# Performance work log

Measured on AMD Instinct MI355X. Metric: run time of the kernel, lower is better.

Reference implementation:

```python
import jax, jax.numpy as jnp
import numpy as np

HID, HEADS = 2048, 16
HD = HID // HEADS  # head_dim = 128
EPS = 1e-6


def rope_tables(head_dim, max_pos, base=10000.0):
    inv = 1.0 / (base ** (jnp.arange(0, head_dim, 2, dtype=jnp.float32) / head_dim))
    t = jnp.arange(max_pos, dtype=jnp.float32)
    freqs = jnp.outer(t, inv)                      # [max_pos, d/2]
    emb = jnp.concatenate([freqs, freqs], axis=-1)  # [max_pos, d]
    return jnp.cos(emb), jnp.sin(emb)


def rotate_half(x):
    x1, x2 = jnp.split(x, 2, axis=-1)
    return jnp.concatenate([-x2, x1], axis=-1)


def lf_gate(x, c1w, c1b, c2w, c2b, rms_w):
    # x: [b, s, h]; prompt phase -> lf1/lf2 caches are zeros -> zero-pad 1 step on time axis
    xt = jnp.transpose(x, (0, 2, 1))[..., None]                 # [b, h, s, 1]
    xt = jnp.pad(xt, ((0, 0), (0, 0), (1, 0), (0, 0)))           # [b, h, s+1, 1]
    dn = ('NCHW', 'OIHW', 'NCHW')
    o1 = jax.lax.conv_general_dilated(xt, c1w, (1, 1), 'VALID', dimension_numbers=dn)
    o1 = o1 + c1b[None, :, None, None]                           # [b, h/2, s, 1]
    o1 = jnp.pad(o1, ((0, 0), (0, 0), (1, 0), (0, 0)))           # [b, h/2, s+1, 1]
    o2 = jax.lax.conv_general_dilated(o1, c2w, (1, 1), 'VALID', dimension_numbers=dn)
    o2 = o2 + c2b[None, :, None, None]                           # [b, h, s, 1]
    y = jnp.transpose(o2[..., 0], (0, 2, 1)) + x                 # residual, [b, s, h]
    var = jnp.mean(y * y, axis=-1, keepdims=True)
    return y * jax.lax.rsqrt(var + EPS) * rms_w


def setup_inputs() -> dict:
    key = jax.random.key(0)
    ks = jax.random.split(key, 10)
    b, s = 2, 2048
    inp = {
        'hidden_states': jax.random.normal(ks[0], (b, s, HID), jnp.float32),
        'positions': jnp.arange(s, dtype=jnp.int32),
        'wq': jax.random.normal(ks[1], (HID, HID), jnp.float32) * 0.02,
        'wk': jax.random.normal(ks[2], (HID, HID), jnp.float32) * 0.02,
        'wv': jax.random.normal(ks[3], (HID, HID), jnp.float32) * 0.02,
        'wo': jax.random.normal(ks[4], (HID, HID), jnp.float32) * 0.02,
        'conv1_w': jax.random.normal(ks[5], (HID // 2, HID, 2, 1), jnp.float32) * 0.02,
        'conv1_b': jnp.zeros((HID // 2,), jnp.float32),
        'conv2_w': jax.random.normal(ks[6], (HID, HID // 2, 2, 1), jnp.float32) * 0.02,
        'conv2_b': jnp.zeros((HID,), jnp.float32),
        'rms_w': jnp.ones((HID,), jnp.float32),
    }
    return inp


def reference(hidden_states, positions, wq, wk, wv, wo, conv1_w, conv1_b, conv2_w, conv2_b, rms_w):
    b, s, _ = hidden_states.shape
    # value projection from raw hidden states (pre-gate)
    v = (hidden_states @ wv).reshape(b, s, HEADS, HD)            # [b, s, H, d]
    # localized-filtering gate (prompt phase: zero caches)
    h = lf_gate(hidden_states, conv1_w, conv1_b, conv2_w, conv2_b, rms_w)
    q = h @ wq                                                   # [b, s, H*d]
    k = h @ wk
    # faithful Yuan quirk: concat q,k then reshape to [b,s,H,2d] and chunk
    qk = jnp.concatenate([q, k], axis=-1).reshape(b, s, HEADS, 2 * HD)
    q, k = jnp.split(qk, 2, axis=-1)                             # each [b, s, H, d]
    # rotary
    cos, sin = rope_tables(HD, 8192)
    c = cos[positions][None, :, None, :]                         # [1, s, 1, d]
    sn = sin[positions][None, :, None, :]
    q = q * c + rotate_half(q) * sn
    k = k * c + rotate_half(k) * sn
    # causal attention (paged attention reduces to this for the prompt)
    scale = HD ** -0.5
    scores = jnp.einsum('bqhd,bkhd->bhqk', q, k) * scale         # [b, H, s, s]
    mask = jnp.tril(jnp.ones((s, s), dtype=bool))
    scores = jnp.where(mask[None, None], scores, jnp.finfo(scores.dtype).min)
    probs = jax.nn.softmax(scores, axis=-1)
    out = jnp.einsum('bhqk,bkhd->bqhd', probs, v).reshape(b, s, HEADS * HD)
    return out @ wo
```

## Files before the change

### kernel.cpp

```cpp
#include <hip/hip_runtime.h>

#define HID 2048
#define HEADS 16
#define HD 128
#define BATCH 2
#define S 2048
#define ROWS (BATCH*S)

typedef short short8 __attribute__((ext_vector_type(8)));
typedef unsigned short ushort4v __attribute__((ext_vector_type(4)));
typedef unsigned short ushort2v __attribute__((ext_vector_type(2)));
typedef float f32x4 __attribute__((ext_vector_type(4)));
typedef __bf16 bf16x8 __attribute__((ext_vector_type(8)));
typedef __bf16 bf16x4 __attribute__((ext_vector_type(4)));

static __device__ __forceinline__ float b2f(unsigned short u) {
  union { float f; unsigned int i; } v; v.i = ((unsigned int)u) << 16; return v.f;
}
static __device__ __forceinline__ unsigned short f2b(float f) {
  union { float f; unsigned int i; } v; v.f = f;
  unsigned int u = v.i;
  unsigned int r = ((u >> 16) & 1u) + 0x7fffu;
  return (unsigned short)((u + r) >> 16);
}

static __device__ __forceinline__ void gload_lds16(const unsigned short* g, unsigned short* l) {
  __builtin_amdgcn_global_load_lds(
      (const __attribute__((address_space(1))) unsigned int*)(const void*)g,
      (__attribute__((address_space(3))) unsigned int*)(void*)l,
      16, 0, 0);
}

__global__ void fill_debug(unsigned short* __restrict__ out, long n) {
  long i = (long)blockIdx.x * blockDim.x + threadIdx.x;
  if (i < n) out[i] = 0x447A;
}

__global__ void prep_all(const float* __restrict__ c1w, const float* __restrict__ c2w,
                         const float* __restrict__ x, const int* __restrict__ positions,
                         const float* __restrict__ c1b, const float* __restrict__ c2b,
                         const float* __restrict__ rmsw,
                         unsigned short* __restrict__ w1t0, unsigned short* __restrict__ w1t1,
                         unsigned short* __restrict__ w2t0, unsigned short* __restrict__ w2t1,
                         unsigned short* __restrict__ xb,
                         float* __restrict__ ctab, float* __restrict__ stab,
                         unsigned short* __restrict__ c1bb, unsigned short* __restrict__ c2bb,
                         unsigned short* __restrict__ rmswb, unsigned short* __restrict__ zpg) {
  int job = blockIdx.y;
  if (job == 0 || job == 1) {
    const float* w = (job == 0) ? c1w : c2w;
    unsigned short* o0 = (job == 0) ? w1t0 : w2t0;
    unsigned short* o1 = (job == 0) ? w1t1 : w2t1;
    long i = (long)blockIdx.x * 256 + threadIdx.x;
    f32x4 v = *(const f32x4*)(w + i*4);
    ushort2v a = { f2b(v[0]), f2b(v[2]) };
    ushort2v b = { f2b(v[1]), f2b(v[3]) };
    *(ushort2v*)(o0 + i*2) = a;
    *(ushort2v*)(o1 + i*2) = b;
  } else if (job == 2) {
    long i = (long)blockIdx.x * 256 + threadIdx.x;
    #pragma unroll
    for (int rep = 0; rep < 2; ++rep) {
      long idx = i + (long)rep * 1048576L;
      f32x4 v = *(const f32x4*)(x + idx*4);
      ushort4v o = { f2b(v[0]), f2b(v[1]), f2b(v[2]), f2b(v[3]) };
      *(ushort4v*)(xb + idx*4) = o;
    }
  } else {
    int bx = blockIdx.x;
    if (bx < 512) {
      int t = bx * 4 + (threadIdx.x >> 6);
      int i = threadIdx.x & 63;
      float pos = (float)positions[t];
      float inv = powf(10000.0f, -(float)i / 64.0f);
      float ang = pos * inv;
      float sv, cv;
      sincosf(ang, &sv, &cv);
      ctab[t*64 + i] = cv;
      stab[t*64 + i] = sv;
    } else if (bx < 544) {
      int i = (bx - 512) * 256 + threadIdx.x;
      if (i < 1024) c1bb[i] = f2b(c1b[i]);
      if (i < 2048) { c2bb[i] = f2b(c2b[i]); rmswb[i] = f2b(rmsw[i]); }
      zpg[i] = 0;
    }
  }
}

__global__ void transpose4(const float* __restrict__ s0, const float* __restrict__ s1,
                           const float* __restrict__ s2, const float* __restrict__ s3,
                           unsigned short* __restrict__ d0, unsigned short* __restrict__ d1,
                           unsigned short* __restrict__ d2, unsigned short* __restrict__ d3) {
  __shared__ unsigned short tl[64][73];
  const float* in; unsigned short* out; int perm;
  switch (blockIdx.z) {
    case 0:  in = s0; out = d0; perm = 1; break;
    case 1:  in = s1; out = d1; perm = 1; break;
    case 2:  in = s2; out = d2; perm = 0; break;
    default: in = s3; out = d3; perm = 0; break;
  }
  int n0 = blockIdx.x * 64, k0 = blockIdx.y * 64;
  int tid = threadIdx.x;
  int r = tid >> 3, c8 = (tid & 7) * 8;
  #pragma unroll
  for (int j = 0; j < 2; ++j) {
    int rr = r + j*32;
    const float* p = in + (size_t)(k0 + rr)*HID + n0 + c8;
    f32x4 v0 = *(const f32x4*)p;
    f32x4 v1 = *(const f32x4*)(p + 4);
    #pragma unroll
    for (int e = 0; e < 4; ++e) { tl[rr][c8 + e] = f2b(v0[e]); tl[rr][c8 + 4 + e] = f2b(v1[e]); }
  }
  __syncthreads();
  #pragma unroll
  for (int j = 0; j < 2; ++j) {
    int rr = r + j*32;
    int orow = n0 + rr;
    if (perm) {
      int s5 = (orow >> 5) & 3;
      s5 = (s5 == 1) ? 2 : (s5 == 2) ? 1 : s5;
      orow = (orow & ~127) | (s5 << 5) | (orow & 31);
    }
    short8 v;
    #pragma unroll
    for (int e = 0; e < 8; ++e) v[e] = (short)tl[c8 + e][rr];
    *(short8*)(out + (size_t)orow*HID + k0 + c8) = v;
  }
}


static __device__ __forceinline__ int swz_scol(int lane) {
  return (((lane & 7) * 16) ^ (((lane >> 3) & 7) << 4)) >> 1;
}

static __device__ __forceinline__ void rd_af(const unsigned short* Ah, bf16x8 (&afr)[4][2],
                                             int wm, int lr, int col0, int axor) {
  #pragma unroll
  for (int mi = 0; mi < 4; ++mi) {
    const unsigned short* rp = Ah + (wm*64 + mi*16 + lr) * 64;
    #pragma unroll
    for (int kk = 0; kk < 2; ++kk)
      afr[mi][kk] = *(const bf16x8*)(rp + (((kk*64 + col0) ^ axor) >> 1));
  }
}
static __device__ __forceinline__ void rd_bf(const unsigned short* Bh, bf16x8 (&bfr)[2][2],
                                             int wn, int lr, int col0, int axor) {
  #pragma unroll
  for (int ni = 0; ni < 2; ++ni) {
    const unsigned short* rp = Bh + (wn*32 + ni*16 + lr) * 64;
    #pragma unroll
    for (int kk = 0; kk < 2; ++kk)
      bfr[ni][kk] = *(const bf16x8*)(rp + (((kk*64 + col0) ^ axor) >> 1));
  }
}
static __device__ __forceinline__ void mfma16(const bf16x8 (&afr)[4][2], const bf16x8 (&bfr)[2][2],
                                              f32x4 (&ac)[4][2]) {
  #pragma unroll
  for (int kk = 0; kk < 2; ++kk)
    #pragma unroll
    for (int mi = 0; mi < 4; ++mi)
      #pragma unroll
      for (int ni = 0; ni < 2; ++ni)
        ac[mi][ni] = __builtin_amdgcn_mfma_f32_16x16x32_bf16(afr[mi][kk], bfr[ni][kk], ac[mi][ni], 0, 0, 0);
}


struct SPtrs { const unsigned short* p[6]; };

static __device__ __forceinline__ void build_ptrs(SPtrs& sp,
    const unsigned short* Ap, const unsigned short* Bp, int Ksz, int sh,
    int m0, int n0, const unsigned short* zpg, int tid) {
  int lane = tid & 63;
  int scol = swz_scol(lane);
  #pragma unroll
  for (int j = 0; j < 2; ++j) {
    int row = ((tid >> 6) * 2 + j) * 8 + (lane >> 3);
    int gr = m0 + row;
    sp.p[j]     = (sh && ((gr & (S - 1)) == 0)) ? (zpg + scol)
                                                : (Ap + (size_t)(gr - sh)*Ksz + scol);
    sp.p[2 + j] = Bp + (size_t)(n0 + row)*Ksz + scol;
    sp.p[4 + j] = Bp + (size_t)(n0 + 128 + row)*Ksz + scol;
  }
}

static __device__ __forceinline__ void stage6(unsigned short* buf, SPtrs& sp, int tid) {
  int c0 = (tid >> 6) * 1024;
  gload_lds16(sp.p[0], buf + c0);
  gload_lds16(sp.p[1], buf + c0 + 512);
  gload_lds16(sp.p[2], buf + 8192  + c0);
  gload_lds16(sp.p[3], buf + 8192  + c0 + 512);
  gload_lds16(sp.p[4], buf + 16384 + c0);
  gload_lds16(sp.p[5], buf + 16384 + c0 + 512);
  #pragma unroll
  for (int i = 0; i < 6; ++i) sp.p[i] += 64;
}

static __device__ __forceinline__ void gemm8_core(
    unsigned short* lds,
    const unsigned short* __restrict__ A1, const unsigned short* __restrict__ A2,
    const unsigned short* __restrict__ B1, const unsigned short* __restrict__ B2,
    int K1, int K2,
    const unsigned short* __restrict__ bias, const unsigned short* __restrict__ resid,
    void* __restrict__ Cout, int outmode, int N, int m0, int n0,
    int a1shift, const unsigned short* __restrict__ zrow) {
  int tid = threadIdx.x;
  int lane = tid & 63, w = tid >> 6;
  int wm = w >> 2, wn = w & 3;
  int lr = lane & 15, g = lane >> 4;
  int col0 = g * 16;
  int axor = (lr & 7) << 4;
  int nk1 = K1 >> 6;
  int nk = (K1 + K2) >> 6;
  f32x4 acc[2][4][2] = {};
  bf16x8 afr[4][2], bfr0[2][2], bfr1[2][2];

  unsigned short* buf0 = lds;
  unsigned short* buf1 = lds + 24576;
  unsigned short* buf2 = lds + 49152;

  SPtrs sp;
  build_ptrs(sp, A1, B1, K1, a1shift, m0, n0, zrow, tid);

  stage6(buf0, sp, tid);
  stage6(buf1, sp, tid);

  unsigned short* cur = buf0;
  unsigned short* nx1 = buf1;
  unsigned short* nx2 = buf2;
  for (int t = 0; t < nk; ++t) {
    if (t < nk - 1) asm volatile("s_waitcnt vmcnt(6)" ::: "memory");
    else            asm volatile("s_waitcnt vmcnt(0)" ::: "memory");
    __builtin_amdgcn_s_barrier();
    asm volatile("" ::: "memory");

    rd_af(cur,         afr,  wm, lr, col0, axor);
    rd_bf(cur + 8192,  bfr0, wn, lr, col0, axor);
    rd_bf(cur + 16384, bfr1, wn, lr, col0, axor);
    if (t + 2 < nk) {
      if (t + 2 == nk1) build_ptrs(sp, A2, B2, K2, 0, m0, n0, zrow, tid);
      stage6(nx2, sp, tid);
    }
    __builtin_amdgcn_s_setprio(1);
    mfma16(afr, bfr0, acc[0]);
    mfma16(afr, bfr1, acc[1]);
    __builtin_amdgcn_s_setprio(0);

    unsigned short* tmp = cur; cur = nx1; nx1 = nx2; nx2 = tmp;
  }

  #pragma unroll
  for (int qn = 0; qn < 2; ++qn)
    #pragma unroll
    for (int mi = 0; mi < 4; ++mi) {
      int row0 = m0 + wm*64 + mi*16 + g*4;
      #pragma unroll
      for (int ni = 0; ni < 2; ++ni) {
        int col = n0 + qn*128 + wn*32 + ni*16 + lr;
        float bv = bias ? b2f(bias[col]) : 0.f;
        f32x4 a = acc[qn][mi][ni];
        #pragma unroll
        for (int j = 0; j < 4; ++j) {
          size_t idx = (size_t)(row0 + j) * N + col;
          float v = a[j] + bv;
          if (resid) v += b2f(resid[idx]);
          if (outmode == 1) ((float*)Cout)[idx] = v;
          else ((unsigned short*)Cout)[idx] = f2b(v);
        }
      }
    }
}

template<int SHIFT>
__launch_bounds__(512, 1)
__global__ void gemm8_bt(const unsigned short* __restrict__ A1,
                         const unsigned short* __restrict__ A2,
                         const unsigned short* __restrict__ B1,
                         const unsigned short* __restrict__ B2,
                         int K1, int K2,
                         const unsigned short* __restrict__ bias,
                         const unsigned short* __restrict__ resid,
                         void* __restrict__ Cout, int outmode, int N,
                         const unsigned short* __restrict__ zrow) {
  __shared__ __align__(16) unsigned short lds[73728];
  gemm8_core(lds, A1, A2, B1, B2, K1, K2, bias, resid, Cout, outmode, N,
             blockIdx.x*128, blockIdx.y*256, SHIFT, zrow);
}

struct HPtr { const unsigned short* p0; const unsigned short* p1; };
static __device__ __forceinline__ void hinit(HPtr& h, const unsigned short* base,
                                             int row0, int tid) {
  int lane = tid & 63;
  int scol = swz_scol(lane);
  int r0 = ((tid >> 6) * 2) * 8 + (lane >> 3);
  h.p0 = base + (size_t)(row0 + r0) * 2048 + scol;
  h.p1 = base + (size_t)(row0 + r0 + 8) * 2048 + scol;
}
static __device__ __forceinline__ void hinit_sh(HPtr& h, const unsigned short* base,
                                                int row0, const unsigned short* zpg, int tid) {
  int lane = tid & 63;
  int scol = swz_scol(lane);
  int r0 = ((tid >> 6) * 2) * 8 + (lane >> 3);
  int g0 = row0 + r0, g1 = row0 + r0 + 8;
  h.p0 = ((g0 & (S - 1)) == 0) ? (zpg + scol) : (base + (size_t)(g0 - 1) * 2048 + scol);
  h.p1 = ((g1 & (S - 1)) == 0) ? (zpg + scol) : (base + (size_t)(g1 - 1) * 2048 + scol);
}
static __device__ __forceinline__ void hstage(unsigned short* slot, HPtr& h, int tid) {
  int c0 = (tid >> 6) * 1024;
  gload_lds16(h.p0, slot + c0);
  gload_lds16(h.p1, slot + c0 + 512);
  h.p0 += 64; h.p1 += 64;
}

static __device__ __forceinline__ void gemm256_loop(
    unsigned short* lds, HPtr& hA0, HPtr& hA1, HPtr& hB0, HPtr& hB1,
    f32x4 (&acc)[2][2][4][2], int wm, int wn, int lr, int col0, int axor, int tid) {
  bf16x8 af[4][2], bf0[2][2], bf1[2][2];
  const int nk = 2048 >> 6;
  hstage(lds + 0,             hA0, tid);
  hstage(lds + 8192,          hA1, tid);
  hstage(lds + 16384,         hB0, tid);
  hstage(lds + 24576,         hB1, tid);
  hstage(lds + 32768 + 0,     hA0, tid);
  hstage(lds + 32768 + 16384, hB0, tid);
  hstage(lds + 32768 + 24576, hB1, tid);
  asm volatile("s_waitcnt vmcnt(6)" ::: "memory");
  __builtin_amdgcn_s_barrier();
  asm volatile("" ::: "memory");

  for (int t = 0; t < nk; ++t) {
    unsigned short* cur = lds + (t & 1) * 32768;
    unsigned short* oth = lds + ((t & 1) ^ 1) * 32768;

    rd_af(cur,         af,  wm, lr, col0, axor);
    rd_bf(cur + 16384, bf0, wn, lr, col0, axor);
    if (t + 1 < nk) hstage(oth + 8192, hA1, tid);
    __builtin_amdgcn_s_barrier();
    asm volatile("s_waitcnt lgkmcnt(0)" ::: "memory");
    __builtin_amdgcn_s_setprio(1);
    mfma16(af, bf0, acc[0][0]);
    __builtin_amdgcn_s_setprio(0);
    __builtin_amdgcn_s_barrier();

    rd_bf(cur + 24576, bf1, wn, lr, col0, axor);
    if (t + 2 < nk) hstage(cur, hA0, tid);
    __builtin_amdgcn_s_barrier();
    asm volatile("s_waitcnt lgkmcnt(0)" ::: "memory");
    __builtin_amdgcn_s_setprio(1);
    mfma16(af, bf1, acc[0][1]);
    __builtin_amdgcn_s_setprio(0);
    __builtin_amdgcn_s_barrier();

    rd_af(cur + 8192, af, wm, lr, col0, axor);
    if (t + 2 < nk) hstage(cur + 16384, hB0, tid);
    __builtin_amdgcn_s_barrier();
    asm volatile("s_waitcnt lgkmcnt(0)" ::: "memory");
    __builtin_amdgcn_s_setprio(1);
    mfma16(af, bf1, acc[1][1]);
    __builtin_amdgcn_s_setprio(0);
    __builtin_amdgcn_s_barrier();

    if (t + 2 < nk) hstage(cur + 24576, hB1, tid);
    __builtin_amdgcn_s_barrier();
    asm volatile("s_waitcnt lgkmcnt(0)" ::: "memory");
    __builtin_amdgcn_s_setprio(1);
    mfma16(af, bf0, acc[1][0]);
    __builtin_amdgcn_s_setprio(0);
    if (t + 2 < nk) asm volatile("s_waitcnt vmcnt(6)" ::: "memory");
    else            asm volatile("s_waitcnt vmcnt(0)" ::: "memory");
    __builtin_amdgcn_s_barrier();
    asm volatile("" ::: "memory");
  }
}

__launch_bounds__(512, 1)
__global__ void gemm256_bt(const unsigned short* __restrict__ A,
                           const unsigned short* __restrict__ B,
                           unsigned short* __restrict__ C, int N) {
  __shared__ __align__(16) unsigned short lds[65536];
  int tid = threadIdx.x;
  int lane = tid & 63, w = tid >> 6;
  int wm = w >> 2, wn = w & 3;
  int lr = lane & 15, g = lane >> 4;
  int col0 = g * 16;
  int axor = (lr & 7) << 4;
  int nwg = gridDim.x * gridDim.y;
  int lin = blockIdx.y * gridDim.x + blockIdx.x;
  int cpx = nwg >> 3;
  int swz = (lin & 7) * cpx + (lin >> 3);
  int m0 = (swz % gridDim.x) * 256, n0 = (swz / gridDim.x) * 256;
  f32x4 acc[2][2][4][2] = {};

  HPtr hA0, hA1, hB0, hB1;
  hinit(hA0, A, m0,       tid);
  hinit(hA1, A, m0 + 128, tid);
  hinit(hB0, B, n0,       tid);
  hinit(hB1, B, n0 + 128, tid);
  gemm256_loop(lds, hA0, hA1, hB0, hB1, acc, wm, wn, lr, col0, axor, tid);

  #pragma unroll
  for (int qm = 0; qm < 2; ++qm)
    #pragma unroll
    for (int mi = 0; mi < 4; ++mi) {
      int row0 = m0 + qm*128 + wm*64 + mi*16 + g*4;
      #pragma unroll
      for (int qn = 0; qn < 2; ++qn)
        #pragma unroll
        for (int ni = 0; ni < 2; ++ni) {
          int col = n0 + qn*128 + wn*32 + ni*16 + lr;
          f32x4 a = acc[qm][qn][mi][ni];
          #pragma unroll
          for (int j = 0; j < 4; ++j)
            C[(size_t)(row0 + j) * N + col] = f2b(a[j]);
        }
    }
}

__launch_bounds__(512, 1)
__global__ void gemm256_trio(const unsigned short* __restrict__ xb,
                             const unsigned short* __restrict__ w1t0,
                             const unsigned short* __restrict__ w1t1,
                             const unsigned short* __restrict__ wvt,
                             unsigned short* __restrict__ o1a,
                             unsigned short* __restrict__ o1b,
                             unsigned short* __restrict__ vtg,
                             const unsigned short* __restrict__ zpg) {
  __shared__ __align__(16) unsigned short lds[65536];
  int tid = threadIdx.x;
  int lane = tid & 63, w = tid >> 6;
  int wm = w >> 2, wn = w & 3;
  int lr = lane & 15, g = lane >> 4;
  int col0 = g * 16;
  int axor = (lr & 7) << 4;
  int lin = blockIdx.x;
  int swz = (lin & 7) * 32 + (lin >> 3);
  int job, s;
  if (swz < 64)       { job = 0; s = swz; }
  else if (swz < 128) { job = 1; s = swz - 64; }
  else                { job = 2; s = swz - 128; }
  int m0 = (s & 15) * 256;
  int n0 = (s >> 4) * 256;
  f32x4 acc[2][2][4][2] = {};

  HPtr hA0, hA1, hB0, hB1;
  if (job == 0) { hinit_sh(hA0, xb, m0, zpg, tid); hinit_sh(hA1, xb, m0 + 128, zpg, tid); }
  else          { hinit(hA0, xb, m0, tid);         hinit(hA1, xb, m0 + 128, tid); }
  const unsigned short* B = (job == 0) ? w1t0 : (job == 1) ? w1t1 : wvt;
  hinit(hB0, B, n0,       tid);
  hinit(hB1, B, n0 + 128, tid);
  gemm256_loop(lds, hA0, hA1, hB0, hB1, acc, wm, wn, lr, col0, axor, tid);

  if (job < 2) {
    unsigned short* C = (job == 0) ? o1a : o1b;
    #pragma unroll
    for (int qm = 0; qm < 2; ++qm)
      #pragma unroll
      for (int mi = 0; mi < 4; ++mi) {
        int row0 = m0 + qm*128 + wm*64 + mi*16 + g*4;
        #pragma unroll
        for (int qn = 0; qn < 2; ++qn)
          #pragma unroll
          for (int ni = 0; ni < 2; ++ni) {
            int col = n0 + qn*128 + wn*32 + ni*16 + lr;
            f32x4 a = acc[qm][qn][mi][ni];
            #pragma unroll
            for (int j = 0; j < 4; ++j)
              C[(size_t)(row0 + j) * 1024 + col] = f2b(a[j]);
          }
      }
  } else {
    #pragma unroll
    for (int qm = 0; qm < 2; ++qm)
      #pragma unroll
      for (int mi = 0; mi < 4; ++mi) {
        int row0 = m0 + qm*128 + wm*64 + mi*16 + g*4;
        int bb = row0 >> 11;
        int s0 = row0 & (S - 1);
        #pragma unroll
        for (int qn = 0; qn < 2; ++qn)
          #pragma unroll
          for (int ni = 0; ni < 2; ++ni) {
            int col = n0 + qn*128 + wn*32 + ni*16 + lr;
            size_t base = ((size_t)bb * HID + col) * S + s0;
            f32x4 a = acc[qm][qn][mi][ni];
            ushort4v pk;
            #pragma unroll
            for (int j = 0; j < 4; ++j) pk[j] = f2b(a[j]);
            *(ushort4v*)(vtg + base) = pk;
          }
      }
  }
}

__global__ void add_bias(const unsigned short* __restrict__ a,
                         const unsigned short* __restrict__ b,
                         const unsigned short* __restrict__ bias,
                         unsigned short* __restrict__ o) {
  long i8 = ((long)blockIdx.x * 256 + threadIdx.x) * 8;
  short8 va = *(const short8*)(a + i8);
  short8 vb = *(const short8*)(b + i8);
  short8 wb = *(const short8*)(bias + (i8 & 1023));
  short8 vo;
  #pragma unroll
  for (int e = 0; e < 8; ++e)
    vo[e] = (short)f2b(b2f((unsigned short)va[e]) + b2f((unsigned short)vb[e])
                       + b2f((unsigned short)wb[e]));
  *(short8*)(o + i8) = vo;
}

__global__ void rmsnorm_rows(const unsigned short* __restrict__ y,
                             const unsigned short* __restrict__ w,
                             unsigned short* __restrict__ out) {
  int r = blockIdx.x;
  int c8 = threadIdx.x * 8;
  const unsigned short* yr = y + (size_t)r * HID;
  short8 v = *(const short8*)(yr + c8);
  float f[8];
  float ss = 0.f;
  #pragma unroll
  for (int e = 0; e < 8; ++e) { f[e] = b2f((unsigned short)v[e]); ss += f[e]*f[e]; }
  #pragma unroll
  for (int o = 32; o; o >>= 1) ss += __shfl_xor(ss, o);
  __shared__ float red[4];
  if ((threadIdx.x & 63) == 0) red[threadIdx.x >> 6] = ss;
  __syncthreads();
  float tot = red[0] + red[1] + red[2] + red[3];
  float scale = rsqrtf(tot / (float)HID + 1e-6f);
  short8 wv = *(const short8*)(w + c8);
  short8 o8;
  #pragma unroll
  for (int e = 0; e < 8; ++e) o8[e] = (short)f2b(f[e] * scale * b2f((unsigned short)wv[e]));
  *(short8*)(out + (size_t)r*HID + c8) = o8;
}

__global__ void rope_rearrange(const unsigned short* __restrict__ qkf,
                               const float* __restrict__ ctab, const float* __restrict__ stab,
                               unsigned short* __restrict__ qr, unsigned short* __restrict__ kr) {
  int r = blockIdx.x;
  int t = r & (S - 1);
  int h = threadIdx.x >> 4;
  int i4 = (threadIdx.x & 15) * 4;
  int pc = (i4 & 31) + ((i4 >> 5) << 6);
  const unsigned short* qk = qkf + (size_t)r * (2*HID) + h * 256;
  f32x4 c = *(const f32x4*)(ctab + t*64 + i4);
  f32x4 s = *(const f32x4*)(stab + t*64 + i4);
  ushort4v q1 = *(const ushort4v*)(qk + pc);
  ushort4v q2 = *(const ushort4v*)(qk + pc + 32);
  ushort4v k1 = *(const ushort4v*)(qk + 128 + pc);
  ushort4v k2 = *(const ushort4v*)(qk + 128 + pc + 32);
  size_t o = (size_t)r * HID + (size_t)h * HD;
  const float SC = 0.08838834764831845f * 1.44269504088896340f;
  ushort4v oq1, oq2, ok1, ok2;
  #pragma unroll
  for (int e = 0; e < 4; ++e) {
    float a = b2f(q1[e]), b = b2f(q2[e]);
    float x = b2f(k1[e]), y = b2f(k2[e]);
    oq1[e] = f2b((a*c[e] - b*s[e]) * SC);
    oq2[e] = f2b((b*c[e] + a*s[e]) * SC);
    ok1[e] = f2b(x*c[e] - y*s[e]);
    ok2[e] = f2b(y*c[e] + x*s[e]);
  }
  *(ushort4v*)(qr + o + i4)      = oq1;
  *(ushort4v*)(qr + o + 64 + i4) = oq2;
  *(ushort4v*)(kr + o + i4)      = ok1;
  *(ushort4v*)(kr + o + 64 + i4) = ok2;
}

#define KT 64

static __device__ __forceinline__ void attn_pass(
    int qt, int b, int h, unsigned short* lds,
    const unsigned short* __restrict__ Qr, const unsigned short* __restrict__ Kr,
    const unsigned short* __restrict__ Vt, unsigned short* __restrict__ Out) {
  int tid = threadIdx.x, lane = tid & 63, w = tid >> 6;
  int q0 = qt * 64;
  size_t bS = (size_t)b * S;
  size_t ho = (size_t)h * HD;
  int lr = lane & 15, g = lane >> 4;
  int rsw = (lane & 7) << 3;
  __syncthreads();
  bf16x8 bq[4];
  {
    int qrow = q0 + w*16 + lr;
    const unsigned short* qp = Qr + (bS + qrow)*HID + ho + g*8;
    #pragma unroll
    for (int kk = 0; kk < 4; ++kk) bq[kk] = *(const bf16x8*)(qp + kk*32);
  }
  const unsigned short* kp[4];
  const unsigned short* vp[4];
  #pragma unroll
  for (int j = 0; j < 4; ++j) {
    int c = w*4 + j;
    int rk = c*4 + (lane >> 4);
    int sck = ((lane & 15) * 8) ^ ((rk & 7) << 3);
    kp[j] = Kr + (bS + rk)*HID + ho + sck;
    int rv = c*8 + (lane >> 3);
    int scv = ((lane & 7) * 8) ^ ((rv & 7) << 3);
    vp[j] = Vt + ((size_t)b*HID + ho + rv)*S + scv;
  }
  int cdst = (w*4) * 512;
  unsigned short* curK = lds;
  unsigned short* curV = lds + 8192;
  unsigned short* nxtK = lds + 16384;
  unsigned short* nxtV = lds + 24576;
  #pragma unroll
  for (int j = 0; j < 4; ++j) {
    gload_lds16(kp[j], curK + cdst + j*512);
    gload_lds16(vp[j], curV + cdst + j*512);
    kp[j] += (size_t)KT * HID;
    vp[j] += KT;
  }
  f32x4 o[8] = {};
  float m = -1e30f, l = 0.f;
  unsigned short* PlW = lds + 32768 + w*1024;
  int ntiles = qt + 1;
  for (int kt = 0; kt < ntiles; ++kt) {
    asm volatile("s_waitcnt vmcnt(0)" ::: "memory");
    __builtin_amdgcn_s_barrier();
    asm volatile("" ::: "memory");
    if (kt + 1 < ntiles) {
      #pragma unroll
      for (int j = 0; j < 4; ++j) {
        gload_lds16(kp[j], nxtK + cdst + j*512);
        gload_lds16(vp[j], nxtV + cdst + j*512);
        kp[j] += (size_t)KT * HID;
        vp[j] += KT;
      }
    }
    f32x4 st[4] = {};
    __builtin_amdgcn_s_setprio(1);
    #pragma unroll
    for (int kk = 0; kk < 4; ++kk) {
      #pragma unroll
      for (int mi = 0; mi < 4; ++mi) {
        bf16x8 a = *(const bf16x8*)(&curK[(mi*16 + lr)*128 + ((kk*32 + g*8) ^ rsw)]);
        st[mi] = __builtin_amdgcn_mfma_f32_16x16x32_bf16(a, bq[kk], st[mi], 0, 0, 0);
      }
    }
    __builtin_amdgcn_s_setprio(0);
    bool lastt = (kt == ntiles - 1);
    float tm = -1e30f;
    #pragma unroll
    for (int mi = 0; mi < 4; ++mi)
      #pragma unroll
      for (int r = 0; r < 4; ++r) {
        float v = st[mi][r];
        if (lastt && (mi*16 + 4*g + r) > (w*16 + lr)) v = -1e30f;
        st[mi][r] = v;
        tm = fmaxf(tm, v);
      }
    tm = fmaxf(tm, __shfl_xor(tm, 16));
    tm = fmaxf(tm, __shfl_xor(tm, 32));
    if (!__all(tm - m <= 11.5f)) {
      float mn = fmaxf(m, tm);
      float sc = exp2f(m - mn);
      float s0 = __shfl(sc, 4*g+0), s1 = __shfl(sc, 4*g+1);
      float s2 = __shfl(sc, 4*g+2), s3 = __shfl(sc, 4*g+3);
      #pragma unroll
      for (int ni = 0; ni < 8; ++ni) {
        o[ni][0] *= s0; o[ni][1] *= s1; o[ni][2] *= s2; o[ni][3] *= s3;
      }
      l *= sc;
      m = mn;
    }
    float ts = 0.f;
    __bf16 pbf[4][4];
    #pragma unroll
    for (int mi = 0; mi < 4; ++mi)
      #pragma unroll
      for (int r = 0; r < 4; ++r) {
        float p = exp2f(st[mi][r] - m);
        ts += p;
        pbf[mi][r] = (__bf16)p;
      }
    ts += __shfl_xor(ts, 16);
    ts += __shfl_xor(ts, 32);
    l += ts;
    #pragma unroll
    for (int mi = 0; mi < 4; ++mi) {
      bf16x4 pk = { pbf[mi][0], pbf[mi][1], pbf[mi][2], pbf[mi][3] };
      *(bf16x4*)(&PlW[lr*64 + ((mi*16 + 4*g) ^ rsw)]) = pk;
    }
    asm volatile("" ::: "memory");
    __builtin_amdgcn_s_setprio(1);
    #pragma unroll
    for (int kk = 0; kk < 2; ++kk) {
      int pc = (kk*32 + g*8) ^ rsw;
      bf16x8 a = *(const bf16x8*)(&PlW[lr*64 + pc]);
      #pragma unroll
      for (int ni = 0; ni < 8; ++ni) {
        bf16x8 bv = *(const bf16x8*)(&curV[(ni*16 + lr)*64 + pc]);
        o[ni] = __builtin_amdgcn_mfma_f32_16x16x32_bf16(a, bv, o[ni], 0, 0, 0);
      }
    }
    __builtin_amdgcn_s_setprio(0);
    unsigned short* t0 = curK; curK = nxtK; nxtK = t0;
    unsigned short* t1 = curV; curV = nxtV; nxtV = t1;
  }
  float l0 = __shfl(l, 4*g+0), l1 = __shfl(l, 4*g+1);
  float l2 = __shfl(l, 4*g+2), l3 = __shfl(l, 4*g+3);
  float i0 = 1.f/l0, i1 = 1.f/l1, i2 = 1.f/l2, i3 = 1.f/l3;
  int rbase = q0 + w*16 + 4*g;
  #pragma unroll
  for (int ni = 0; ni < 8; ++ni) {
    size_t cbase = ho + ni*16 + lr;
    Out[(bS + rbase + 0)*HID + cbase] = f2b(o[ni][0]*i0);
    Out[(bS + rbase + 1)*HID + cbase] = f2b(o[ni][1]*i1);
    Out[(bS + rbase + 2)*HID + cbase] = f2b(o[ni][2]*i2);
    Out[(bS + rbase + 3)*HID + cbase] = f2b(o[ni][3]*i3);
  }
}

__launch_bounds__(256, 2)
__global__ void attn_mfma(const unsigned short* __restrict__ Qr,
                          const unsigned short* __restrict__ Kr,
                          const unsigned short* __restrict__ Vt,
                          unsigned short* __restrict__ Out) {
  __shared__ __align__(16) unsigned short lds[36864];
  int bh = blockIdx.x;
  int b = bh >> 4, h = bh & 15;
  int by = blockIdx.y;
  attn_pass(31 - by, b, h, lds, Qr, Kr, Vt, Out);
  attn_pass(by,      b, h, lds, Qr, Kr, Vt, Out);
}

extern "C" void kernel_launch(void* const* d_in, const int* in_sizes, int n_in,
                              void* d_out, int out_size, void* d_ws, size_t ws_size,
                              hipStream_t stream) {
  const float* x_raw   = (const float*)d_in[0];
  const int* positions = (const int*)d_in[1];
  const float* wq_raw  = (const float*)d_in[2];
  const float* wk_raw  = (const float*)d_in[3];
  const float* wv_raw  = (const float*)d_in[4];
  const float* wo_raw  = (const float*)d_in[5];
  const float* c1w_raw = (const float*)d_in[6];
  const float* c1b_raw = (const float*)d_in[7];
  const float* c2w_raw = (const float*)d_in[8];
  const float* c2b_raw = (const float*)d_in[9];
  const float* rms_raw = (const float*)d_in[10];

  const size_t WS_NEEDED = 140000000;
  if (ws_size < WS_NEEDED) {
    long n = (long)out_size;
    fill_debug<<<dim3((unsigned)((n + 255) / 256)), dim3(256), 0, stream>>>((unsigned short*)d_out, n);
    return;
  }

  char* ws = (char*)d_ws;
  size_t off = 0;
  auto alloc = [&](size_t bytes) { char* p = ws + off; off += (bytes + 255) & ~(size_t)255; return p; };
  float* ctab          = (float*)alloc((size_t)S*64*4);
  float* stab          = (float*)alloc((size_t)S*64*4);
  unsigned short* wqkt = (unsigned short*)alloc((size_t)2*HID*HID*2);
  unsigned short* wvt  = (unsigned short*)alloc((size_t)HID*HID*2);
  unsigned short* wot  = (unsigned short*)alloc((size_t)HID*HID*2);
  unsigned short* w1t0 = (unsigned short*)alloc((size_t)1024*HID*2);
  unsigned short* w1t1 = (unsigned short*)alloc((size_t)1024*HID*2);
  unsigned short* w2t0 = (unsigned short*)alloc((size_t)HID*1024*2);
  unsigned short* w2t1 = (unsigned short*)alloc((size_t)HID*1024*2);
  unsigned short* xb   = (unsigned short*)alloc((size_t)ROWS*HID*2);
  unsigned short* qrb  = (unsigned short*)alloc((size_t)ROWS*HID*2);
  unsigned short* o1   = (unsigned short*)alloc((size_t)ROWS*1024*2);
  unsigned short* yb   = (unsigned short*)alloc((size_t)ROWS*HID*2);
  unsigned short* hg   = (unsigned short*)alloc((size_t)ROWS*HID*2);
  unsigned short* qkf  = (unsigned short*)alloc((size_t)ROWS*2*HID*2);
  unsigned short* vtg  = (unsigned short*)alloc((size_t)BATCH*HID*S*2);
  unsigned short* c1bb = (unsigned short*)alloc(1024*2);
  unsigned short* c2bb = (unsigned short*)alloc(2048*2);
  unsigned short* rmswb= (unsigned short*)alloc(2048*2);
  unsigned short* zpg  = (unsigned short*)alloc(8192*2);
  unsigned short* krr  = xb;
  unsigned short* attn = yb;
  unsigned short* o1a  = qkf;
  unsigned short* o1b  = qkf + (size_t)ROWS*1024;

  dim3 b256(256);
  dim3 b512(512);
  prep_all<<<dim3(4096, 4), b256, 0, stream>>>(c1w_raw, c2w_raw, x_raw, positions,
                                               c1b_raw, c2b_raw, rms_raw,
                                               w1t0, w1t1, w2t0, w2t1, xb,
                                               ctab, stab, c1bb, c2bb, rmswb, zpg);
  transpose4<<<dim3(32,32,4), b256, 0, stream>>>(wq_raw, wk_raw, wv_raw, wo_raw,
                                                 wqkt, wqkt + (size_t)HID*HID, wvt, wot);
  gemm256_trio<<<dim3(256), b512, 0, stream>>>(xb, w1t0, w1t1, wvt, o1a, o1b, vtg, zpg);
  add_bias<<<dim3(ROWS*1024/8/256), b256, 0, stream>>>(o1a, o1b, c1bb, o1);
  gemm8_bt<1><<<dim3(ROWS/128, HID/256), b512, 0, stream>>>(o1, o1, w2t0, w2t1, 1024, 1024, c2bb, xb, yb, 0, HID, zpg);
  rmsnorm_rows<<<dim3(ROWS), b256, 0, stream>>>(yb, rmswb, hg);
  gemm256_bt<<<dim3(ROWS/256, (2*HID)/256), b512, 0, stream>>>(hg, wqkt, qkf, 2*HID);
  rope_rearrange<<<dim3(ROWS), b256, 0, stream>>>(qkf, ctab, stab, qrb, krr);
  attn_mfma<<<dim3(BATCH*HEADS, 16), b256, 0, stream>>>(qrb, krr, vtg, attn);
  gemm8_bt<0><<<dim3(ROWS/128, HID/256), b512, 0, stream>>>(attn, attn, wot, wot, HID, 0, nullptr, nullptr, d_out, 1, HID, nullptr);
}
```

Baseline: 348.8 us.

## Split conv2 GEMM into two 256x256-tile GEMMs and fuse reduction into RMSNorm

Replaces the 128x256-tile conv2 GEMM, which accumulated both shifted and unshifted K-halves in one kernel, with a 256-block 256x256-tile kernel. That kernel runs the two halves as separate jobs and writes two partial outputs. The RMSNorm kernel now sums the partials, the bias and the residual before normalizing, so the epilogue work of the old GEMM moves there. The intent is better MFMA tile efficiency and full-GPU parallelism, at the cost of writing and re-reading an extra bf16 partial buffer and rounding each partial to bf16.

```diff
diff --git a/kernel.cpp b/kernel.cpp
--- a/kernel.cpp
+++ b/kernel.cpp
@@ -288,21 +288,22 @@
 
 struct HPtr { const unsigned short* p0; const unsigned short* p1; };
 static __device__ __forceinline__ void hinit(HPtr& h, const unsigned short* base,
-                                             int row0, int tid) {
+                                             int row0, int Ksz, int tid) {
   int lane = tid & 63;
   int scol = swz_scol(lane);
   int r0 = ((tid >> 6) * 2) * 8 + (lane >> 3);
-  h.p0 = base + (size_t)(row0 + r0) * 2048 + scol;
-  h.p1 = base + (size_t)(row0 + r0 + 8) * 2048 + scol;
+  h.p0 = base + (size_t)(row0 + r0) * Ksz + scol;
+  h.p1 = base + (size_t)(row0 + r0 + 8) * Ksz + scol;
 }
 static __device__ __forceinline__ void hinit_sh(HPtr& h, const unsigned short* base,
-                                                int row0, const unsigned short* zpg, int tid) {
+                                                int row0, int Ksz,
+                                                const unsigned short* zpg, int tid) {
   int lane = tid & 63;
   int scol = swz_scol(lane);
   int r0 = ((tid >> 6) * 2) * 8 + (lane >> 3);
   int g0 = row0 + r0, g1 = row0 + r0 + 8;
-  h.p0 = ((g0 & (S - 1)) == 0) ? (zpg + scol) : (base + (size_t)(g0 - 1) * 2048 + scol);
-  h.p1 = ((g1 & (S - 1)) == 0) ? (zpg + scol) : (base + (size_t)(g1 - 1) * 2048 + scol);
+  h.p0 = ((g0 & (S - 1)) == 0) ? (zpg + scol) : (base + (size_t)(g0 - 1) * Ksz + scol);
+  h.p1 = ((g1 & (S - 1)) == 0) ? (zpg + scol) : (base + (size_t)(g1 - 1) * Ksz + scol);
 }
 static __device__ __forceinline__ void hstage(unsigned short* slot, HPtr& h, int tid) {
   int c0 = (tid >> 6) * 1024;
@@ -311,11 +312,12 @@
   h.p0 += 64; h.p1 += 64;
 }
 
+template<int NKT>
 static __device__ __forceinline__ void gemm256_loop(
     unsigned short* lds, HPtr& hA0, HPtr& hA1, HPtr& hB0, HPtr& hB1,
     f32x4 (&acc)[2][2][4][2], int wm, int wn, int lr, int col0, int axor, int tid) {
   bf16x8 af[4][2], bf0[2][2], bf1[2][2];
-  const int nk = 2048 >> 6;
+  const int nk = NKT;
   hstage(lds + 0,             hA0, tid);
   hstage(lds + 8192,          hA1, tid);
   hstage(lds + 16384,         hB0, tid);
@@ -391,11 +393,11 @@
   f32x4 acc[2][2][4][2] = {};
 
   HPtr hA0, hA1, hB0, hB1;
-  hinit(hA0, A, m0,       tid);
-  hinit(hA1, A, m0 + 128, tid);
-  hinit(hB0, B, n0,       tid);
-  hinit(hB1, B, n0 + 128, tid);
-  gemm256_loop(lds, hA0, hA1, hB0, hB1, acc, wm, wn, lr, col0, axor, tid);
+  hinit(hA0, A, m0,       2048, tid);
+  hinit(hA1, A, m0 + 128, 2048, tid);
+  hinit(hB0, B, n0,       2048, tid);
+  hinit(hB1, B, n0 + 128, 2048, tid);
+  gemm256_loop<32>(lds, hA0, hA1, hB0, hB1, acc, wm, wn, lr, col0, axor, tid);
 
   #pragma unroll
   for (int qm = 0; qm < 2; ++qm)
@@ -442,12 +444,12 @@
   f32x4 acc[2][2][4][2] = {};
 
   HPtr hA0, hA1, hB0, hB1;
-  if (job == 0) { hinit_sh(hA0, xb, m0, zpg, tid); hinit_sh(hA1, xb, m0 + 128, zpg, tid); }
-  else          { hinit(hA0, xb, m0, tid);         hinit(hA1, xb, m0 + 128, tid); }
+  if (job == 0) { hinit_sh(hA0, xb, m0, 2048, zpg, tid); hinit_sh(hA1, xb, m0 + 128, 2048, zpg, tid); }
+  else          { hinit(hA0, xb, m0, 2048, tid);         hinit(hA1, xb, m0 + 128, 2048, tid); }
   const unsigned short* B = (job == 0) ? w1t0 : (job == 1) ? w1t1 : wvt;
-  hinit(hB0, B, n0,       tid);
-  hinit(hB1, B, n0 + 128, tid);
-  gemm256_loop(lds, hA0, hA1, hB0, hB1, acc, wm, wn, lr, col0, axor, tid);
+  hinit(hB0, B, n0,       2048, tid);
+  hinit(hB1, B, n0 + 128, 2048, tid);
+  gemm256_loop<32>(lds, hA0, hA1, hB0, hB1, acc, wm, wn, lr, col0, axor, tid);
 
   if (job < 2) {
     unsigned short* C = (job == 0) ? o1a : o1b;
@@ -491,6 +493,55 @@
   }
 }
 
+__launch_bounds__(512, 1)
+__global__ void gemm256_duo(const unsigned short* __restrict__ o1,
+                            const unsigned short* __restrict__ w2t0,
+                            const unsigned short* __restrict__ w2t1,
+                            unsigned short* __restrict__ pA,
+                            unsigned short* __restrict__ pB,
+                            const unsigned short* __restrict__ zpg) {
+  __shared__ __align__(16) unsigned short lds[65536];
+  int tid = threadIdx.x;
+  int lane = tid & 63, w = tid >> 6;
+  int wm = w >> 2, wn = w & 3;
+  int lr = lane & 15, g = lane >> 4;
+  int col0 = g * 16;
+  int axor = (lr & 7) << 4;
+  int lin = blockIdx.x;
+  int swz = (lin & 7) * 32 + (lin >> 3);
+  int job = swz >> 7;
+  int s = swz & 127;
+  int m0 = (s & 15) * 256;
+  int n0 = (s >> 4) * 256;
+  f32x4 acc[2][2][4][2] = {};
+
+  HPtr hA0, hA1, hB0, hB1;
+  if (job == 0) { hinit_sh(hA0, o1, m0, 1024, zpg, tid); hinit_sh(hA1, o1, m0 + 128, 1024, zpg, tid); }
+  else          { hinit(hA0, o1, m0, 1024, tid);         hinit(hA1, o1, m0 + 128, 1024, tid); }
+  const unsigned short* B = (job == 0) ? w2t0 : w2t1;
+  hinit(hB0, B, n0,       1024, tid);
+  hinit(hB1, B, n0 + 128, 1024, tid);
+  gemm256_loop<16>(lds, hA0, hA1, hB0, hB1, acc, wm, wn, lr, col0, axor, tid);
+
+  unsigned short* C = (job == 0) ? pA : pB;
+  #pragma unroll
+  for (int qm = 0; qm < 2; ++qm)
+    #pragma unroll
+    for (int mi = 0; mi < 4; ++mi) {
+      int row0 = m0 + qm*128 + wm*64 + mi*16 + g*4;
+      #pragma unroll
+      for (int qn = 0; qn < 2; ++qn)
+        #pragma unroll
+        for (int ni = 0; ni < 2; ++ni) {
+          int col = n0 + qn*128 + wn*32 + ni*16 + lr;
+          f32x4 a = acc[qm][qn][mi][ni];
+          #pragma unroll
+          for (int j = 0; j < 4; ++j)
+            C[(size_t)(row0 + j) * HID + col] = f2b(a[j]);
+        }
+    }
+}
+
 __global__ void add_bias(const unsigned short* __restrict__ a,
                          const unsigned short* __restrict__ b,
                          const unsigned short* __restrict__ bias,
@@ -507,17 +558,27 @@
   *(short8*)(o + i8) = vo;
 }
 
-__global__ void rmsnorm_rows(const unsigned short* __restrict__ y,
-                             const unsigned short* __restrict__ w,
-                             unsigned short* __restrict__ out) {
+__global__ void rms_fuse(const unsigned short* __restrict__ pA,
+                         const unsigned short* __restrict__ pB,
+                         const unsigned short* __restrict__ bias,
+                         const unsigned short* __restrict__ resid,
+                         const unsigned short* __restrict__ w,
+                         unsigned short* __restrict__ out) {
   int r = blockIdx.x;
   int c8 = threadIdx.x * 8;
-  const unsigned short* yr = y + (size_t)r * HID;
-  short8 v = *(const short8*)(yr + c8);
+  size_t base = (size_t)r * HID + c8;
+  short8 va = *(const short8*)(pA + base);
+  short8 vb = *(const short8*)(pB + base);
+  short8 vx = *(const short8*)(resid + base);
+  short8 vbi = *(const short8*)(bias + c8);
   float f[8];
   float ss = 0.f;
   #pragma unroll
-  for (int e = 0; e < 8; ++e) { f[e] = b2f((unsigned short)v[e]); ss += f[e]*f[e]; }
+  for (int e = 0; e < 8; ++e) {
+    f[e] = b2f((unsigned short)va[e]) + b2f((unsigned short)vb[e])
+         + b2f((unsigned short)vbi[e]) + b2f((unsigned short)vx[e]);
+    ss += f[e]*f[e];
+  }
   #pragma unroll
   for (int o = 32; o; o >>= 1) ss += __shfl_xor(ss, o);
   __shared__ float red[4];
@@ -529,7 +590,7 @@
   short8 o8;
   #pragma unroll
   for (int e = 0; e < 8; ++e) o8[e] = (short)f2b(f[e] * scale * b2f((unsigned short)wv[e]));
-  *(short8*)(out + (size_t)r*HID + c8) = o8;
+  *(short8*)(out + base) = o8;
 }
 
 __global__ void rope_rearrange(const unsigned short* __restrict__ qkf,
@@ -772,6 +833,8 @@
   unsigned short* attn = yb;
   unsigned short* o1a  = qkf;
   unsigned short* o1b  = qkf + (size_t)ROWS*1024;
+  unsigned short* cpA  = qkf;
+  unsigned short* cpB  = qkf + (size_t)ROWS*HID;
 
   dim3 b256(256);
   dim3 b512(512);
@@ -783,8 +846,8 @@
                                                  wqkt, wqkt + (size_t)HID*HID, wvt, wot);
   gemm256_trio<<<dim3(256), b512, 0, stream>>>(xb, w1t0, w1t1, wvt, o1a, o1b, vtg, zpg);
   add_bias<<<dim3(ROWS*1024/8/256), b256, 0, stream>>>(o1a, o1b, c1bb, o1);
-  gemm8_bt<1><<<dim3(ROWS/128, HID/256), b512, 0, stream>>>(o1, o1, w2t0, w2t1, 1024, 1024, c2bb, xb, yb, 0, HID, zpg);
-  rmsnorm_rows<<<dim3(ROWS), b256, 0, stream>>>(yb, rmswb, hg);
+  gemm256_duo<<<dim3(256), b512, 0, stream>>>(o1, w2t0, w2t1, cpA, cpB, zpg);
+  rms_fuse<<<dim3(ROWS), b256, 0, stream>>>(cpA, cpB, c2bb, xb, rmswb, hg);
   gemm256_bt<<<dim3(ROWS/256, (2*HID)/256), b512, 0, stream>>>(hg, wqkt, qkf, 2*HID);
   rope_rearrange<<<dim3(ROWS), b256, 0, stream>>>(qkf, ctab, stab, qrb, krr);
   attn_mfma<<<dim3(BATCH*HEADS, 16), b256, 0, stream>>>(qrb, krr, vtg, attn);
```

Result: faster. 339.1 us (-2.8%).
